# Performance work log

Hardware: AMD Instinct MI355X
Metric: run time of the kernel (lower is better)

The kernel has to match this reference:

```python
import jax, jax.numpy as jnp
import numpy as np

QUANT_BLOCK = 32  # GGUF Q4_0-style block size
QUANT_ZERO = 8.0  # 4-bit codes are offset-binary around 8


def setup_inputs() -> dict:
    key = jax.random.key(0)
    k_x, k_q, k_s, k_up, k_dn, k_b = jax.random.split(key, 6)
    O, I, R = 4096, 4096, 16
    T = 2048  # tokens (batch*seq)
    x = jax.random.normal(k_x, (T, I), dtype=jnp.float32)
    # quantized 4-bit codes stored unpacked as int32 in [0, 16)
    q = jax.random.randint(k_q, (O, I), 0, 16, dtype=jnp.int32)
    # per-block scales (small positive, like real GGUF d values)
    scales = jax.random.uniform(k_s, (O, I // QUANT_BLOCK), dtype=jnp.float32) * 0.05
    lora_up = jax.random.normal(k_up, (O, R), dtype=jnp.float32) * 0.02
    lora_down = jax.random.normal(k_dn, (R, I), dtype=jnp.float32) * 0.02
    alpha = jnp.ones((), dtype=jnp.float32)
    bias = jax.random.normal(k_b, (O,), dtype=jnp.float32)
    return {"x": x, "q": q, "scales": scales, "lora_up": lora_up,
            "lora_down": lora_down, "alpha": alpha, "bias": bias}


def _dequant(q, scales):
    # q: [O, I] int codes; scales: [O, I/BLOCK] per-block scale
    O, I = q.shape
    qf = q.reshape(O, I // QUANT_BLOCK, QUANT_BLOCK).astype(scales.dtype)
    w = (qf - QUANT_ZERO) * scales[:, :, None]  # [O, I/B, B]
    return w.reshape(O, I)


def reference(x, q, scales, lora_up, lora_down, alpha, bias):
    # on-the-fly dequant (GGMLLayer.get_weight -> dequantize_tensor)
    W = _dequant(q, scales)  # [O, I]
    # LoRA patch apply (ray_calculate_weight): W += alpha * up @ down
    W = W + alpha * jnp.einsum('or,ri->oi', lora_up, lora_down)
    # linear forward: y = x @ W^T + b
    return jnp.einsum('ti,oi->to', x, W) + bias
```

## Files before the change

### kernel.cpp

```cpp
#include <hip/hip_runtime.h>
#include <hip/hip_bf16.h>
#include <stdint.h>

#define T_DIM 2048
#define I_DIM 4096
#define O_DIM 4096
#define R_DIM 16
#define QBLK  32

typedef __bf16 bf16x8 __attribute__((ext_vector_type(8)));
typedef float  floatx4 __attribute__((ext_vector_type(4)));
typedef unsigned short ushort_t;

#define AS1 __attribute__((address_space(1)))
#define AS3 __attribute__((address_space(3)))

__device__ __forceinline__ ushort_t f2bf(float f) {
  unsigned u = __float_as_uint(f);
  u += 0x7FFFu + ((u >> 16) & 1u);
  return (ushort_t)(u >> 16);
}

__device__ __forceinline__ float dot4(float4 a, float4 b) {
  return a.x * b.x + a.y * b.y + a.z * b.z + a.w * b.w;
}

__global__ __launch_bounds__(256) void k_prep(const float* __restrict__ x,
                                              const int* __restrict__ q,
                                              const float* __restrict__ scales,
                                              const float* __restrict__ down,
                                              const float* __restrict__ alphap,
                                              ushort_t* __restrict__ xb,
                                              ushort_t* __restrict__ wb,
                                              float* __restrict__ xd) {
  __shared__ float ds[16 * 512];
  const int b = blockIdx.x, tid = threadIdx.x;

  if (b < 4096) {
    int idx = b * 256 + tid;
    const float4* xp = (const float4*)x;
    float4 a = xp[idx * 2], c = xp[idx * 2 + 1];
    union { ushort_t u[8]; uint4 v; } r;
    r.u[0] = f2bf(a.x); r.u[1] = f2bf(a.y); r.u[2] = f2bf(a.z); r.u[3] = f2bf(a.w);
    r.u[4] = f2bf(c.x); r.u[5] = f2bf(c.y); r.u[6] = f2bf(c.z); r.u[7] = f2bf(c.w);
    ((uint4*)xb)[idx] = r.v;
    return;
  }
  if (b < 12288) {
    int idx = (b - 4096) * 256 + tid;
    int o  = idx >> 9;
    int i0 = (idx & 511) * 8;
    float s = scales[o * (I_DIM / QBLK) + (i0 >> 5)];
    const int4* qp = (const int4*)(q + (size_t)o * I_DIM + i0);
    int4 q0 = qp[0], q1 = qp[1];
    union { ushort_t u[8]; uint4 v; } r;
    r.u[0] = f2bf((float)(q0.x - 8) * s); r.u[1] = f2bf((float)(q0.y - 8) * s);
    r.u[2] = f2bf((float)(q0.z - 8) * s); r.u[3] = f2bf((float)(q0.w - 8) * s);
    r.u[4] = f2bf((float)(q1.x - 8) * s); r.u[5] = f2bf((float)(q1.y - 8) * s);
    r.u[6] = f2bf((float)(q1.z - 8) * s); r.u[7] = f2bf((float)(q1.w - 8) * s);
    ((uint4*)wb)[idx] = r.v;
    return;
  }
  {
    const int blk = b - 12288;
    const int tl = tid >> 5, s = tid & 31;
    const int t = blk * 8 + tl;
    float acc[16];
#pragma unroll
    for (int r = 0; r < 16; ++r) acc[r] = 0.f;
    for (int c = 0; c < 8; ++c) {
      const int ib = c * 512;
      __syncthreads();
#pragma unroll
      for (int j = 0; j < 8; ++j) {
        int e = j * 256 + tid;
        int r = e >> 7, col = e & 127;
        ((float4*)ds)[e] = ((const float4*)(down + (size_t)r * I_DIM + ib))[col];
      }
      __syncthreads();
#pragma unroll
      for (int j = 0; j < 4; ++j) {
        float4 xv = ((const float4*)(x + (size_t)t * I_DIM + ib))[s + 32 * j];
#pragma unroll
        for (int r = 0; r < 16; ++r) {
          float4 dv = ((const float4*)ds)[r * 128 + s + 32 * j];
          acc[r] += dot4(xv, dv);
        }
      }
    }
    const float al = alphap[0];
#pragma unroll
    for (int r = 0; r < 16; ++r) {
      float v = acc[r];
      v += __shfl_down(v, 16, 32);
      v += __shfl_down(v, 8, 32);
      v += __shfl_down(v, 4, 32);
      v += __shfl_down(v, 2, 32);
      v += __shfl_down(v, 1, 32);
      if (s == 0) xd[t * 16 + r] = v * al;
    }
  }
}

__global__ __launch_bounds__(256) void k_gemm(const ushort_t* __restrict__ xb,
                                              const ushort_t* __restrict__ wb,
                                              const float* __restrict__ bias,
                                              const float* __restrict__ xd,
                                              const float* __restrict__ up,
                                              float* __restrict__ y) {
  __shared__ __align__(16) ushort_t As[128 * 64];
  __shared__ __align__(16) ushort_t Bs[64 * 64];
  const int tid = threadIdx.x;
  const int oT = blockIdx.x * 64, tT = blockIdx.y * 128;
  const int lane = tid & 63;
  const int wv = tid >> 6;
  const int wm = wv >> 1, wn = wv & 1;
  const int quad = lane >> 4, m16 = lane & 15;

  floatx4 acc[4][2] = {};

  for (int kt = 0; kt < I_DIM / 64; ++kt) {
    const int k0 = kt * 64;
#pragma unroll
    for (int it = 0; it < 4; ++it) {
      const int seg_base = wv * 256 + it * 64;
      const int seg = seg_base + lane;
      const int r = seg >> 3;
      const int cg = (seg & 7) ^ (r & 7);
      __builtin_amdgcn_global_load_lds(
          (const AS1 char*)(xb + (size_t)(tT + r) * I_DIM + k0 + cg * 8),
          (AS3 char*)(As + seg_base * 8), 16, 0, 0);
    }
#pragma unroll
    for (int it = 0; it < 2; ++it) {
      const int seg_base = wv * 128 + it * 64;
      const int seg = seg_base + lane;
      const int r = seg >> 3;
      const int cg = (seg & 7) ^ (r & 7);
      __builtin_amdgcn_global_load_lds(
          (const AS1 char*)(wb + (size_t)(oT + r) * I_DIM + k0 + cg * 8),
          (AS3 char*)(Bs + seg_base * 8), 16, 0, 0);
    }
    __syncthreads();

#pragma unroll
    for (int ks2 = 0; ks2 < 2; ++ks2) {
      const int c = ks2 * 4 + quad;
      bf16x8 af[4], bfr[2];
#pragma unroll
      for (int im = 0; im < 4; ++im) {
        int m = wm * 64 + im * 16 + m16;
        af[im] = *(const bf16x8*)(As + (m * 8 + (c ^ (m & 7))) * 8);
      }
#pragma unroll
      for (int in_ = 0; in_ < 2; ++in_) {
        int n = wn * 32 + in_ * 16 + m16;
        bfr[in_] = *(const bf16x8*)(Bs + (n * 8 + (c ^ (n & 7))) * 8);
      }
#pragma unroll
      for (int im = 0; im < 4; ++im)
#pragma unroll
        for (int in_ = 0; in_ < 2; ++in_)
          acc[im][in_] = __builtin_amdgcn_mfma_f32_16x16x32_bf16(
              af[im], bfr[in_], acc[im][in_], 0, 0, 0);
    }
    __syncthreads();
  }

#pragma unroll
  for (int im = 0; im < 4; ++im) {
#pragma unroll
    for (int reg = 0; reg < 4; ++reg) {
      int t = tT + wm * 64 + im * 16 + quad * 4 + reg;
      const float4* xr = (const float4*)(xd + t * 16);
      float4 x0 = xr[0], x1 = xr[1], x2 = xr[2], x3 = xr[3];
#pragma unroll
      for (int in_ = 0; in_ < 2; ++in_) {
        int o = oT + wn * 32 + in_ * 16 + m16;
        const float4* ur = (const float4*)(up + (size_t)o * R_DIM);
        float lv = dot4(x0, ur[0]) + dot4(x1, ur[1]) +
                   dot4(x2, ur[2]) + dot4(x3, ur[3]);
        y[(size_t)t * O_DIM + o] = acc[im][in_][reg] + lv + bias[o];
      }
    }
  }
}

extern "C" void kernel_launch(void* const* d_in, const int* in_sizes, int n_in,
                              void* d_out, int out_size, void* d_ws, size_t ws_size,
                              hipStream_t stream) {
  const float* x      = (const float*)d_in[0];
  const int*   q      = (const int*)d_in[1];
  const float* scales = (const float*)d_in[2];
  const float* up     = (const float*)d_in[3];
  const float* down   = (const float*)d_in[4];
  const float* alpha  = (const float*)d_in[5];
  const float* bias   = (const float*)d_in[6];
  float* y = (float*)d_out;

  ushort_t* xb = (ushort_t*)d_ws;
  ushort_t* wb = (ushort_t*)((char*)d_ws + (size_t)T_DIM * I_DIM * 2);
  float*    xd = (float*)((char*)d_ws + (size_t)T_DIM * I_DIM * 2 + (size_t)O_DIM * I_DIM * 2);

  hipLaunchKernelGGL(k_prep, dim3(4096 + 8192 + 256), dim3(256), 0, stream,
                     x, q, scales, down, alpha, xb, wb, xd);
  hipLaunchKernelGGL(k_gemm, dim3(O_DIM / 64, T_DIM / 128), dim3(256), 0, stream,
                     xb, wb, bias, xd, up, y);
}
```

Measured before the change: 465.7 us.

## Prefetch next GEMM k-tile into registers instead of direct global-to-LDS loads

Replaces the synchronous global_load_lds tile loads with register double-buffering. Each iteration stores the previously fetched tile into LDS, issues global loads for the next k-tile, then runs the MFMAs while those loads are in flight. The intent is to hide global memory latency behind compute. The cost is extra VGPRs and an explicit LDS write, and the final iteration makes one wasted wrapped-around load.

```diff
diff --git a/kernel.cpp b/kernel.cpp
--- a/kernel.cpp
+++ b/kernel.cpp
@@ -11,9 +11,6 @@
 typedef __bf16 bf16x8 __attribute__((ext_vector_type(8)));
 typedef float  floatx4 __attribute__((ext_vector_type(4)));
 typedef unsigned short ushort_t;
-
-#define AS1 __attribute__((address_space(1)))
-#define AS3 __attribute__((address_space(3)))
 
 __device__ __forceinline__ ushort_t f2bf(float f) {
   unsigned u = __float_as_uint(f);
@@ -117,30 +114,42 @@
   const int wm = wv >> 1, wn = wv & 1;
   const int quad = lane >> 4, m16 = lane & 15;
 
+  const int r0 = tid >> 3, cg = tid & 7;
+  const int cs = cg ^ (r0 & 7);
+  const ushort_t* gA[4];
+  ushort_t* lA[4];
+#pragma unroll
+  for (int j = 0; j < 4; ++j) {
+    gA[j] = xb + (size_t)(tT + r0 + 32 * j) * I_DIM + cg * 8;
+    lA[j] = As + ((r0 + 32 * j) * 8 + cs) * 8;
+  }
+  const ushort_t* gB[2];
+  ushort_t* lB[2];
+#pragma unroll
+  for (int j = 0; j < 2; ++j) {
+    gB[j] = wb + (size_t)(oT + r0 + 32 * j) * I_DIM + cg * 8;
+    lB[j] = Bs + ((r0 + 32 * j) * 8 + cs) * 8;
+  }
+
   floatx4 acc[4][2] = {};
+  uint4 va[4], vb[2];
+
+#pragma unroll
+  for (int j = 0; j < 4; ++j) va[j] = *(const uint4*)(gA[j]);
+#pragma unroll
+  for (int j = 0; j < 2; ++j) vb[j] = *(const uint4*)(gB[j]);
 
   for (int kt = 0; kt < I_DIM / 64; ++kt) {
-    const int k0 = kt * 64;
-#pragma unroll
-    for (int it = 0; it < 4; ++it) {
-      const int seg_base = wv * 256 + it * 64;
-      const int seg = seg_base + lane;
-      const int r = seg >> 3;
-      const int cg = (seg & 7) ^ (r & 7);
-      __builtin_amdgcn_global_load_lds(
-          (const AS1 char*)(xb + (size_t)(tT + r) * I_DIM + k0 + cg * 8),
-          (AS3 char*)(As + seg_base * 8), 16, 0, 0);
-    }
-#pragma unroll
-    for (int it = 0; it < 2; ++it) {
-      const int seg_base = wv * 128 + it * 64;
-      const int seg = seg_base + lane;
-      const int r = seg >> 3;
-      const int cg = (seg & 7) ^ (r & 7);
-      __builtin_amdgcn_global_load_lds(
-          (const AS1 char*)(wb + (size_t)(oT + r) * I_DIM + k0 + cg * 8),
-          (AS3 char*)(Bs + seg_base * 8), 16, 0, 0);
-    }
+    const int k1 = ((kt + 1) & 63) * 64;
+    __syncthreads();
+#pragma unroll
+    for (int j = 0; j < 4; ++j) *(uint4*)(lA[j]) = va[j];
+#pragma unroll
+    for (int j = 0; j < 2; ++j) *(uint4*)(lB[j]) = vb[j];
+#pragma unroll
+    for (int j = 0; j < 4; ++j) va[j] = *(const uint4*)(gA[j] + k1);
+#pragma unroll
+    for (int j = 0; j < 2; ++j) vb[j] = *(const uint4*)(gB[j] + k1);
     __syncthreads();
 
 #pragma unroll
@@ -164,7 +173,6 @@
           acc[im][in_] = __builtin_amdgcn_mfma_f32_16x16x32_bf16(
               af[im], bfr[in_], acc[im][in_], 0, 0, 0);
     }
-    __syncthreads();
   }
 
 #pragma unroll
```

After: 831.7 us. 1.79x slower.

## Fuse Q4 dequantization into GEMM B-tile loading with register prefetch

Applied to the files above, without the earlier changes.

Removes the separate weight dequant pass and its bf16 weight buffer from the prep kernel. The GEMM now reads int32 codes and scales directly, dequantizes to bf16 in registers and writes the result to swizzled LDS. Global loads switch from direct-to-LDS to register staging with the next k-tile prefetched. This saves the prep pass's write and re-read of the bf16 weight buffer. In exchange, each GEMM block now re-reads the 4-byte codes and repeats the dequant arithmetic for every token tile, and occupancy is constrained by the launch bound of 4.

```diff
diff --git a/kernel.cpp b/kernel.cpp
--- a/kernel.cpp
+++ b/kernel.cpp
@@ -12,26 +12,24 @@
 typedef float  floatx4 __attribute__((ext_vector_type(4)));
 typedef unsigned short ushort_t;
 
-#define AS1 __attribute__((address_space(1)))
-#define AS3 __attribute__((address_space(3)))
-
 __device__ __forceinline__ ushort_t f2bf(float f) {
   unsigned u = __float_as_uint(f);
   u += 0x7FFFu + ((u >> 16) & 1u);
   return (ushort_t)(u >> 16);
 }
 
+__device__ __forceinline__ unsigned pack2bf(float lo, float hi) {
+  return (unsigned)f2bf(lo) | ((unsigned)f2bf(hi) << 16);
+}
+
 __device__ __forceinline__ float dot4(float4 a, float4 b) {
   return a.x * b.x + a.y * b.y + a.z * b.z + a.w * b.w;
 }
 
 __global__ __launch_bounds__(256) void k_prep(const float* __restrict__ x,
-                                              const int* __restrict__ q,
-                                              const float* __restrict__ scales,
                                               const float* __restrict__ down,
                                               const float* __restrict__ alphap,
                                               ushort_t* __restrict__ xb,
-                                              ushort_t* __restrict__ wb,
                                               float* __restrict__ xd) {
   __shared__ float ds[16 * 512];
   const int b = blockIdx.x, tid = threadIdx.x;
@@ -46,23 +44,8 @@
     ((uint4*)xb)[idx] = r.v;
     return;
   }
-  if (b < 12288) {
-    int idx = (b - 4096) * 256 + tid;
-    int o  = idx >> 9;
-    int i0 = (idx & 511) * 8;
-    float s = scales[o * (I_DIM / QBLK) + (i0 >> 5)];
-    const int4* qp = (const int4*)(q + (size_t)o * I_DIM + i0);
-    int4 q0 = qp[0], q1 = qp[1];
-    union { ushort_t u[8]; uint4 v; } r;
-    r.u[0] = f2bf((float)(q0.x - 8) * s); r.u[1] = f2bf((float)(q0.y - 8) * s);
-    r.u[2] = f2bf((float)(q0.z - 8) * s); r.u[3] = f2bf((float)(q0.w - 8) * s);
-    r.u[4] = f2bf((float)(q1.x - 8) * s); r.u[5] = f2bf((float)(q1.y - 8) * s);
-    r.u[6] = f2bf((float)(q1.z - 8) * s); r.u[7] = f2bf((float)(q1.w - 8) * s);
-    ((uint4*)wb)[idx] = r.v;
-    return;
-  }
   {
-    const int blk = b - 12288;
+    const int blk = b - 4096;
     const int tl = tid >> 5, s = tid & 31;
     const int t = blk * 8 + tl;
     float acc[16];
@@ -102,12 +85,11 @@
   }
 }
 
-__global__ __launch_bounds__(256) void k_gemm(const ushort_t* __restrict__ xb,
-                                              const ushort_t* __restrict__ wb,
-                                              const float* __restrict__ bias,
-                                              const float* __restrict__ xd,
-                                              const float* __restrict__ up,
-                                              float* __restrict__ y) {
+__global__ __launch_bounds__(256, 4) void k_gemm(
+    const ushort_t* __restrict__ xb, const int* __restrict__ q,
+    const float* __restrict__ scales, const float* __restrict__ bias,
+    const float* __restrict__ xd, const float* __restrict__ up,
+    float* __restrict__ y) {
   __shared__ __align__(16) ushort_t As[128 * 64];
   __shared__ __align__(16) ushort_t Bs[64 * 64];
   const int tid = threadIdx.x;
@@ -117,30 +99,62 @@
   const int wm = wv >> 1, wn = wv & 1;
   const int quad = lane >> 4, m16 = lane & 15;
 
+  const int rA = tid >> 3, cgA = tid & 7;
+  const int csA = cgA ^ (rA & 7);
+  const ushort_t* gA = xb + (size_t)(tT + rA) * I_DIM + cgA * 8;
+  ushort_t* lA = As + (rA * 8 + csA) * 8;
+
+  const int rB = tid >> 2, c16 = (tid & 3) * 16;
+  const int cs0 = ((c16 >> 3) ^ (rB & 7)), cs1 = (((c16 >> 3) + 1) ^ (rB & 7));
+  const int* gQ = q + (size_t)(oT + rB) * I_DIM + c16;
+  const float* gS = scales + (size_t)(oT + rB) * (I_DIM / QBLK) + (c16 >> 5);
+  ushort_t* lB0 = Bs + (rB * 8 + cs0) * 8;
+  ushort_t* lB1 = Bs + (rB * 8 + cs1) * 8;
+
   floatx4 acc[4][2] = {};
+  uint4 va0, va1, va2, va3;
+  int4  vq0, vq1, vq2, vq3;
+  float vs;
+
+  va0 = *(const uint4*)(gA);
+  va1 = *(const uint4*)(gA + 32 * I_DIM);
+  va2 = *(const uint4*)(gA + 64 * I_DIM);
+  va3 = *(const uint4*)(gA + 96 * I_DIM);
+  vq0 = *(const int4*)(gQ);
+  vq1 = *(const int4*)(gQ + 4);
+  vq2 = *(const int4*)(gQ + 8);
+  vq3 = *(const int4*)(gQ + 12);
+  vs  = *gS;
 
   for (int kt = 0; kt < I_DIM / 64; ++kt) {
-    const int k0 = kt * 64;
-#pragma unroll
-    for (int it = 0; it < 4; ++it) {
-      const int seg_base = wv * 256 + it * 64;
-      const int seg = seg_base + lane;
-      const int r = seg >> 3;
-      const int cg = (seg & 7) ^ (r & 7);
-      __builtin_amdgcn_global_load_lds(
-          (const AS1 char*)(xb + (size_t)(tT + r) * I_DIM + k0 + cg * 8),
-          (AS3 char*)(As + seg_base * 8), 16, 0, 0);
-    }
-#pragma unroll
-    for (int it = 0; it < 2; ++it) {
-      const int seg_base = wv * 128 + it * 64;
-      const int seg = seg_base + lane;
-      const int r = seg >> 3;
-      const int cg = (seg & 7) ^ (r & 7);
-      __builtin_amdgcn_global_load_lds(
-          (const AS1 char*)(wb + (size_t)(oT + r) * I_DIM + k0 + cg * 8),
-          (AS3 char*)(Bs + seg_base * 8), 16, 0, 0);
-    }
+    const int k1 = ((kt + 1) & 63) * 64;
+    __syncthreads();
+    *(uint4*)(lA)        = va0;
+    *(uint4*)(lA + 2048) = va1;
+    *(uint4*)(lA + 4096) = va2;
+    *(uint4*)(lA + 6144) = va3;
+    {
+      uint4 b0, b1;
+      b0.x = pack2bf((float)(vq0.x - 8) * vs, (float)(vq0.y - 8) * vs);
+      b0.y = pack2bf((float)(vq0.z - 8) * vs, (float)(vq0.w - 8) * vs);
+      b0.z = pack2bf((float)(vq1.x - 8) * vs, (float)(vq1.y - 8) * vs);
+      b0.w = pack2bf((float)(vq1.z - 8) * vs, (float)(vq1.w - 8) * vs);
+      b1.x = pack2bf((float)(vq2.x - 8) * vs, (float)(vq2.y - 8) * vs);
+      b1.y = pack2bf((float)(vq2.z - 8) * vs, (float)(vq2.w - 8) * vs);
+      b1.z = pack2bf((float)(vq3.x - 8) * vs, (float)(vq3.y - 8) * vs);
+      b1.w = pack2bf((float)(vq3.z - 8) * vs, (float)(vq3.w - 8) * vs);
+      *(uint4*)(lB0) = b0;
+      *(uint4*)(lB1) = b1;
+    }
+    va0 = *(const uint4*)(gA + k1);
+    va1 = *(const uint4*)(gA + 32 * I_DIM + k1);
+    va2 = *(const uint4*)(gA + 64 * I_DIM + k1);
+    va3 = *(const uint4*)(gA + 96 * I_DIM + k1);
+    vq0 = *(const int4*)(gQ + k1);
+    vq1 = *(const int4*)(gQ + k1 + 4);
+    vq2 = *(const int4*)(gQ + k1 + 8);
+    vq3 = *(const int4*)(gQ + k1 + 12);
+    vs  = *(gS + (k1 >> 5));
     __syncthreads();
 
 #pragma unroll
@@ -164,7 +178,6 @@
           acc[im][in_] = __builtin_amdgcn_mfma_f32_16x16x32_bf16(
               af[im], bfr[in_], acc[im][in_], 0, 0, 0);
     }
-    __syncthreads();
   }
 
 #pragma unroll
@@ -199,11 +212,10 @@
   float* y = (float*)d_out;
 
   ushort_t* xb = (ushort_t*)d_ws;
-  ushort_t* wb = (ushort_t*)((char*)d_ws + (size_t)T_DIM * I_DIM * 2);
-  float*    xd = (float*)((char*)d_ws + (size_t)T_DIM * I_DIM * 2 + (size_t)O_DIM * I_DIM * 2);
-
-  hipLaunchKernelGGL(k_prep, dim3(4096 + 8192 + 256), dim3(256), 0, stream,
-                     x, q, scales, down, alpha, xb, wb, xd);
+  float*    xd = (float*)((char*)d_ws + (size_t)T_DIM * I_DIM * 2);
+
+  hipLaunchKernelGGL(k_prep, dim3(4096 + 256), dim3(256), 0, stream,
+                     x, down, alpha, xb, xd);
   hipLaunchKernelGGL(k_gemm, dim3(O_DIM / 64, T_DIM / 128), dim3(256), 0, stream,
-                     xb, wb, bias, xd, up, y);
-}
+                     xb, q, scales, bias, xd, up, y);
+}
```

Measured after the change: 482.7 us. 1.04x slower.
